# Kernel tuning notes

Hardware: AMD Instinct MI355X
Metric: run time of the kernel (lower is better)

## Reference

```python
import jax, jax.numpy as jnp
import numpy as np

NEG = -10000.0
START, STOP = 4, 5
NT = 6  # 4 emotions + START + STOP
B, T, V = 512, 2048, 100000


def setup_inputs():
    key = jax.random.key(0)
    ks = jax.random.split(key, 7)
    transitions = jax.random.normal(ks[0], (NT, NT), jnp.float32)
    transitions = transitions.at[START, :].set(NEG).at[:, STOP].set(NEG)
    weight_for_emo_shift = jax.random.normal(ks[1], (4,), jnp.float32)
    multiplier = jax.random.normal(ks[2], (4, 4), jnp.float32)
    multiplier = multiplier.at[jnp.arange(4), jnp.arange(4)].set(NEG)
    out_table = jax.random.normal(ks[3], (V, 4), jnp.float32)
    bias = jax.random.uniform(ks[4], (B, T), jnp.float32)
    sentence = jax.random.randint(ks[5], (B, T), 0, V)
    tags = jax.random.randint(ks[6], (B, T), 0, 4)
    return {"transitions": transitions, "weight_for_emo_shift": weight_for_emo_shift,
            "multiplier": multiplier, "out_table": out_table, "bias": bias,
            "sentence": sentence, "tags": tags}


def _feats(out_table, sentence):
    # sentence: [T] int -> feats [T, 6]; cols 0..3 from out_table lookup,
    # col 4 = +3 at first turn else -3, col 5 = +3 at last turn else -3.
    t = sentence.shape[0]
    emo = out_table[sentence]                                      # [T,4]
    col4 = jnp.full((t,), -3.0, out_table.dtype).at[0].set(3.0)
    col5 = jnp.full((t,), -3.0, out_table.dtype).at[t - 1].set(3.0)
    return jnp.concatenate([emo, col4[:, None], col5[:, None]], axis=1)


def _nll_one(transitions, w, M, feats, bias, tags):
    # CRF forward algorithm (log-partition) minus gold path score for one dialog.
    t = feats.shape[0]

    def step(alpha, inp):
        feat, b = inp                                              # feat [6], b scalar
        shift = b * jnp.tanh((b - 0.5) * w)                        # [4]
        te = transitions.at[:4, :4].add(M * shift[None, :])        # [next, prev]
        alpha = jax.nn.logsumexp(alpha[None, :] + te, axis=1) + feat
        return alpha, None

    alpha0 = jnp.full((NT,), NEG, feats.dtype).at[START].set(0.0)
    alphaT, _ = jax.lax.scan(step, alpha0, (feats, bias))
    fwd = jax.nn.logsumexp(alphaT + transitions[STOP])

    # gold score
    prev = jnp.concatenate([jnp.array([START], tags.dtype), tags[:-1]])
    pc = jnp.clip(prev, 0, 3)
    ar = jnp.arange(t)
    shift = bias[:, None] * jnp.tanh((bias[:, None] - 0.5) * w[None, :])  # [T,4]
    biased = shift[ar, pc] * M[tags, pc]
    use_bias = (tags < 4) & (prev < 4)
    trans_s = transitions[tags, prev] + jnp.where(use_bias, biased, 0.0)
    gold = jnp.sum(trans_s + feats[ar, tags]) + transitions[STOP, tags[-1]]
    return fwd - gold


def reference(transitions, weight_for_emo_shift, multiplier, out_table, bias, sentence, tags):
    # multiplier: softmax over dim 0, then diagonal forced to -1 (as in the
    # in-place .data mutations in the original loop).
    M = jax.nn.softmax(multiplier, axis=0)
    M = M.at[jnp.arange(4), jnp.arange(4)].set(-1.0)
    feats = jax.vmap(lambda s: _feats(out_table, s))(sentence)     # [B,T,6]
    nll = jax.vmap(lambda f, b, tg: _nll_one(transitions, weight_for_emo_shift, M, f, b, tg))(feats, bias, tags)
    return nll                                                     # [B]
```

## Files before the change

### kernel.cpp

```cpp
#include <hip/hip_runtime.h>

#define TT 2048
#define BB 512

typedef float f2 __attribute__((ext_vector_type(2)));
__device__ __forceinline__ f2 mk2(float v){ f2 r; r.x=v; r.y=v; return r; }

#if __has_builtin(__builtin_elementwise_fma)
#define FMA2(a,b,c) __builtin_elementwise_fma((a),(b),(c))
#else
#define FMA2(a,b,c) ((a)*(b)+(c))
#endif

#if __has_builtin(__builtin_amdgcn_exp2f)
__device__ __forceinline__ float fexp2(float x){ return __builtin_amdgcn_exp2f(x); }
#else
__device__ __forceinline__ float fexp2(float x){ return exp2f(x); }
#endif
#if __has_builtin(__builtin_amdgcn_logf)
__device__ __forceinline__ float flog2(float x){ return __builtin_amdgcn_logf(x); }
#else
__device__ __forceinline__ float flog2(float x){ return log2f(x); }
#endif
__device__ __forceinline__ float frcp(float x){ return __builtin_amdgcn_rcpf(x); }

#if __has_builtin(__builtin_amdgcn_cvt_pk_fp8_f32) && __has_builtin(__builtin_amdgcn_cvt_pk_f32_fp8)
__device__ __forceinline__ unsigned enc_lo(float a,float b,unsigned old){
  return (unsigned)__builtin_amdgcn_cvt_pk_fp8_f32(a,b,(int)old,false);
}
__device__ __forceinline__ unsigned enc_hi(float a,float b,unsigned old){
  return (unsigned)__builtin_amdgcn_cvt_pk_fp8_f32(a,b,(int)old,true);
}
__device__ __forceinline__ f2 dec_lo2(unsigned w){
  auto r=__builtin_amdgcn_cvt_pk_f32_fp8((int)w,false); f2 o; o.x=r[0]; o.y=r[1]; return o;
}
__device__ __forceinline__ f2 dec_hi2(unsigned w){
  auto r=__builtin_amdgcn_cvt_pk_f32_fp8((int)w,true); f2 o; o.x=r[0]; o.y=r[1]; return o;
}
#else
__device__ __forceinline__ unsigned enc1(float x){
  if (!(x > 0x1p-10f)) return 0u;
  unsigned b = __float_as_uint(x) + 0x80000u;
  int e = (int)((b>>23)&0xFF) - 127;
  if (e < -6){ int m = (int)(x*512.0f + 0.5f); return (unsigned)m; }
  if (e > 8) return 0x7Eu;
  return (unsigned)(((e+7)<<3) | ((b>>20)&7));
}
__device__ __forceinline__ float dec1(unsigned byte){
  unsigned e=(byte>>3)&0xF, m=byte&7;
  if (e==0) return (float)m * 0x1p-9f;
  return __uint_as_float(((e+120u)<<23)|(m<<20));
}
__device__ __forceinline__ unsigned enc_lo(float a,float b,unsigned old){
  return (old & 0xFFFF0000u) | enc1(a) | (enc1(b)<<8);
}
__device__ __forceinline__ unsigned enc_hi(float a,float b,unsigned old){
  return (old & 0x0000FFFFu) | (enc1(a)<<16) | (enc1(b)<<24);
}
__device__ __forceinline__ f2 dec_lo2(unsigned w){ f2 o; o.x=dec1(w&0xFF); o.y=dec1((w>>8)&0xFF); return o; }
__device__ __forceinline__ f2 dec_hi2(unsigned w){ f2 o; o.x=dec1((w>>16)&0xFF); o.y=dec1(w>>24); return o; }
#endif

__device__ __forceinline__ float lse2_4(float x0,float x1,float x2,float x3){
  float m = fmaxf(fmaxf(x0,x1),fmaxf(x2,x3));
  float e = fexp2(x0-m)+fexp2(x1-m)+fexp2(x2-m)+fexp2(x3-m);
  return m + flog2(e);
}

__global__ __launch_bounds__(256) void crf_part(
    const float* __restrict__ trans,
    const float* __restrict__ w,
    const float* __restrict__ mult,
    const float* __restrict__ out_table,
    const float* __restrict__ bias,
    const int*   __restrict__ sentence,
    const int*   __restrict__ tags,
    float* __restrict__ partM,
    float* __restrict__ partG)
{
  constexpr float INVLN2 = 1.4426950408889634f;
  const int blk = blockIdx.x;
  const int b   = blk >> 2;
  const int p   = blk & 3;
  const int tid = threadIdx.x;

  __shared__ __align__(16) char  s_te[8192];
  __shared__ float s_PAm[64*16];
  __shared__ float s_PAs[64*4];
  __shared__ float s_M[16];
  __shared__ float s_tr[36];
  __shared__ float s_wgold[4];
  float* s_PBm = (float*)s_te;
  float* s_PBs = (float*)(s_te + 4096);

  float trans2[16]; float t2max = -1e30f;
  #pragma unroll
  for (int i=0;i<4;i++)
    #pragma unroll
    for (int k=0;k<4;k++){
      float v = trans[i*6+k]*INVLN2;
      trans2[i*4+k] = v; t2max = fmaxf(t2max, v);
    }
  const float T144 = t2max + 1.4427f;

  float M[16];
  {
    int l = tid & 15;
    float mv = fexp2(mult[l]*INVLN2);
    float s1 = mv + __shfl_xor(mv, 4);
    float cs = s1 + __shfl_xor(s1, 8);
    float Ml = ((l>>2)==(l&3)) ? -1.f : mv*frcp(cs);
    if (tid < 16) s_M[tid] = Ml;
    int mi = __float_as_int(Ml);
    #pragma unroll
    for (int i=0;i<16;i++)
      M[i] = __int_as_float(__builtin_amdgcn_readlane(mi, i));
  }
  const float wc0=w[0]*2.f*INVLN2, wc1=w[1]*2.f*INVLN2,
              wc2=w[2]*2.f*INVLN2, wc3=w[3]*2.f*INVLN2;
  if (tid<36) s_tr[tid]=trans[tid];
  __syncthreads();

  float gold = 0.f;
  float cts;
  {
    const int t0    = tid<<1;
    const int gbase = b*TT + (p<<9) + t0;
    float2 bb2 = *reinterpret_cast<const float2*>(bias + gbase);
    int2  sen2 = *reinterpret_cast<const int2*>(sentence + gbase);
    int2  tg2  = *reinterpret_cast<const int2*>(tags + gbase);
    float4 ftA = *reinterpret_cast<const float4*>(out_table + (size_t)sen2.x*4);
    float4 ftB = *reinterpret_cast<const float4*>(out_table + (size_t)sen2.y*4);

    int pv0;
    if ((tid & 63)==0) pv0 = (p==0 && t0==0) ? 4 : tags[gbase-1];
    else               pv0 = __shfl_up(tg2.y, 1);

    float ctv[2];
    #pragma unroll
    for (int e=0;e<2;e++){
      const int tl = t0 + e;
      float bb   = e ? bb2.y : bb2.x;
      float4 f4e = e ? ftB   : ftA;
      int tg     = e ? tg2.y : tg2.x;
      int pv     = e ? tg2.x : pv0;

      float bh = bb-0.5f;
      float y0=fexp2(bh*wc0); float sh0=bb*(y0-1.f)*frcp(y0+1.f);
      float y1=fexp2(bh*wc1); float sh1=bb*(y1-1.f)*frcp(y1+1.f);
      float y2=fexp2(bh*wc2); float sh2v=bb*(y2-1.f)*frcp(y2+1.f);
      float y3=fexp2(bh*wc3); float sh3=bb*(y3-1.f)*frcp(y3+1.f);
      float s20=sh0*INVLN2, s21=sh1*INVLN2, s22=sh2v*INVLN2, s23=sh3*INVLN2;
      float f20=f4e.x*INVLN2, f21=f4e.y*INVLN2, f22=f4e.z*INVLN2, f23=f4e.w*INVLN2;

      float ct  = fmaxf(fmaxf(f20,f21),fmaxf(f22,f23)) + T144;
      float off = 8.0f - ct;
      float o0=f20+off, o1=f21+off, o2=f22+off, o3=f23+off;
      float a00=fexp2(fmaf(M[ 0],s20,trans2[ 0]+o0));
      float a01=fexp2(fmaf(M[ 1],s21,trans2[ 1]+o0));
      float a02=fexp2(fmaf(M[ 2],s22,trans2[ 2]+o0));
      float a03=fexp2(fmaf(M[ 3],s23,trans2[ 3]+o0));
      float a10=fexp2(fmaf(M[ 4],s20,trans2[ 4]+o1));
      float a11=fexp2(fmaf(M[ 5],s21,trans2[ 5]+o1));
      float a12=fexp2(fmaf(M[ 6],s22,trans2[ 6]+o1));
      float a13=fexp2(fmaf(M[ 7],s23,trans2[ 7]+o1));
      float a20=fexp2(fmaf(M[ 8],s20,trans2[ 8]+o2));
      float a21=fexp2(fmaf(M[ 9],s21,trans2[ 9]+o2));
      float a22=fexp2(fmaf(M[10],s22,trans2[10]+o2));
      float a23=fexp2(fmaf(M[11],s23,trans2[11]+o2));
      float a30=fexp2(fmaf(M[12],s20,trans2[12]+o3));
      float a31=fexp2(fmaf(M[13],s21,trans2[13]+o3));
      float a32=fexp2(fmaf(M[14],s22,trans2[14]+o3));
      float a33=fexp2(fmaf(M[15],s23,trans2[15]+o3));

      unsigned d0=enc_lo(a00,a10,0u); d0=enc_hi(a20,a30,d0);
      unsigned d1=enc_lo(a01,a11,0u); d1=enc_hi(a21,a31,d1);
      unsigned d2=enc_lo(a02,a12,0u); d2=enc_hi(a22,a32,d2);
      unsigned d3=enc_lo(a03,a13,0u); d3=enc_hi(a23,a33,d3);
      int g = (tl ^ ((tl>>3)&7)) << 4;
      *reinterpret_cast<uint4*>(s_te+g) = make_uint4(d0,d1,d2,d3);
      ctv[e] = ct;

      float term;
      if (pv>=4){
        term = s_tr[tg*6+4];
      } else {
        float shp=(pv==0)?sh0:(pv==1)?sh1:(pv==2)?sh2v:sh3;
        term = s_tr[tg*6+pv] + shp*s_M[tg*4+pv];
      }
      term += (tg==0)?f4e.x:(tg==1)?f4e.y:(tg==2)?f4e.z:f4e.w;
      if (p==3 && tl==511) term += s_tr[30+tg];
      gold += term;
    }
    if (p==0 && tid==0){
      *reinterpret_cast<uint4*>(s_te) = make_uint4(0x38u,0x3800u,0x380000u,0x38000000u);
      ctv[0] = 8.0f;
    }
    cts = ctv[0] + ctv[1];
  }
  #pragma unroll
  for (int off=32; off>0; off>>=1) gold += __shfl_down(gold, off);
  if ((tid & 63)==0) s_wgold[tid>>6] = gold;
  float cpair = cts + __shfl_xor(cts, 1);
  float csum  = cpair + __shfl_xor(cpair, 2);
  __syncthreads();

  {
    int c = tid>>2, j = tid&3;
    int t0c = c<<3;
    int K = c & 7;
    f2 a01, a23;
    a01.x = (j==0)?1.f:0.f; a01.y = (j==1)?1.f:0.f;
    a23.x = (j==2)?1.f:0.f; a23.y = (j==3)?1.f:0.f;
    #pragma unroll
    for (int s=0;s<8;s++){
      int g = ((t0c+s) ^ K) << 4;
      uint4 q = *reinterpret_cast<const uint4*>(s_te + g);
      float p0=a01.x, p1=a01.y, p2=a23.x, p3=a23.y;
      f2 n01 = dec_lo2(q.x)*mk2(p0);
      f2 n23 = dec_hi2(q.x)*mk2(p0);
      n01 = FMA2(dec_lo2(q.y), mk2(p1), n01);
      n23 = FMA2(dec_hi2(q.y), mk2(p1), n23);
      n01 = FMA2(dec_lo2(q.z), mk2(p2), n01);
      n23 = FMA2(dec_hi2(q.z), mk2(p2), n23);
      n01 = FMA2(dec_lo2(q.w), mk2(p3), n01);
      n23 = FMA2(dec_hi2(q.w), mk2(p3), n23);
      a01 = n01; a23 = n23;
    }
    float sum = fmaxf((a01.x+a01.y)+(a23.x+a23.y), 1e-30f);
    float inv = frcp(sum);
    float L = flog2(sum) + csum - 64.0f;
    s_PAm[c*16 + 0*4 + j] = a01.x*inv;
    s_PAm[c*16 + 1*4 + j] = a01.y*inv;
    s_PAm[c*16 + 2*4 + j] = a23.x*inv;
    s_PAm[c*16 + 3*4 + j] = a23.y*inv;
    s_PAs[c*4 + j] = L;
  }
  __syncthreads();

  if (tid < 128){
    int q = tid>>2, j = tid&3;
    const float* Am = s_PAm + (2*q)*16;
    const float* As = s_PAs + (2*q)*4;
    const float* Bm = Am + 16;
    const float* Bs = As + 4;
    float b0=Bs[0], b1=Bs[1], b2=Bs[2], b3=Bs[3];
    float m = fmaxf(fmaxf(b0,b1), fmaxf(b2,b3));
    float a0 = Am[0*4+j]*fexp2(b0-m);
    float a1 = Am[1*4+j]*fexp2(b1-m);
    float a2 = Am[2*4+j]*fexp2(b2-m);
    float a3 = Am[3*4+j]*fexp2(b3-m);
    float c0 = fmaf(Bm[ 0],a0, fmaf(Bm[ 1],a1, fmaf(Bm[ 2],a2, Bm[ 3]*a3)));
    float c1 = fmaf(Bm[ 4],a0, fmaf(Bm[ 5],a1, fmaf(Bm[ 6],a2, Bm[ 7]*a3)));
    float c2 = fmaf(Bm[ 8],a0, fmaf(Bm[ 9],a1, fmaf(Bm[10],a2, Bm[11]*a3)));
    float c3 = fmaf(Bm[12],a0, fmaf(Bm[13],a1, fmaf(Bm[14],a2, Bm[15]*a3)));
    float ssum = fmaxf((c0+c1)+(c2+c3), 1e-37f);
    float inv = frcp(ssum);
    s_PBm[q*16+0*4+j] = c0*inv;
    s_PBm[q*16+1*4+j] = c1*inv;
    s_PBm[q*16+2*4+j] = c2*inv;
    s_PBm[q*16+3*4+j] = c3*inv;
    s_PBs[q*4+j] = m + As[j] + flog2(ssum);
  }
  __syncthreads();

  if (tid < 64){
    float *srcM = s_PBm, *srcS = s_PBs, *dstM = s_PAm, *dstS = s_PAs;
    #pragma unroll 1
    for (int n=16; n>=1; n>>=1){
      if (tid < n*4){
        int q = tid>>2, j = tid&3;
        const float* Am = srcM + (2*q)*16;
        const float* As = srcS + (2*q)*4;
        const float* Bm = Am + 16;
        const float* Bs = As + 4;
        float b0=Bs[0], b1=Bs[1], b2=Bs[2], b3=Bs[3];
        float m = fmaxf(fmaxf(b0,b1), fmaxf(b2,b3));
        float a0 = Am[0*4+j]*fexp2(b0-m);
        float a1 = Am[1*4+j]*fexp2(b1-m);
        float a2 = Am[2*4+j]*fexp2(b2-m);
        float a3 = Am[3*4+j]*fexp2(b3-m);
        float c0 = fmaf(Bm[ 0],a0, fmaf(Bm[ 1],a1, fmaf(Bm[ 2],a2, Bm[ 3]*a3)));
        float c1 = fmaf(Bm[ 4],a0, fmaf(Bm[ 5],a1, fmaf(Bm[ 6],a2, Bm[ 7]*a3)));
        float c2 = fmaf(Bm[ 8],a0, fmaf(Bm[ 9],a1, fmaf(Bm[10],a2, Bm[11]*a3)));
        float c3 = fmaf(Bm[12],a0, fmaf(Bm[13],a1, fmaf(Bm[14],a2, Bm[15]*a3)));
        float ssum = fmaxf((c0+c1)+(c2+c3), 1e-37f);
        float inv = frcp(ssum);
        dstM[q*16+0*4+j] = c0*inv;
        dstM[q*16+1*4+j] = c1*inv;
        dstM[q*16+2*4+j] = c2*inv;
        dstM[q*16+3*4+j] = c3*inv;
        dstS[q*4+j] = m + As[j] + flog2(ssum);
      }
      float* tm;
      tm=srcM; srcM=dstM; dstM=tm;
      tm=srcS; srcS=dstS; dstS=tm;
    }
    const int idx = (b<<2) | p;
    if (tid < 16)      partM[idx*20 + tid] = srcM[tid];
    else if (tid < 20) partM[idx*20 + tid] = srcS[tid-16];
    if (tid == 20)
      partG[idx] = ((s_wgold[0]+s_wgold[1])+(s_wgold[2]+s_wgold[3]));
  }
}

__global__ __launch_bounds__(256) void crf_final(
    const float* __restrict__ trans,
    const float* __restrict__ out_table,
    const int*   __restrict__ sentence,
    const float* __restrict__ partM,
    const float* __restrict__ partG,
    float* __restrict__ out)
{
  constexpr float INVLN2 = 1.4426950408889634f;
  constexpr float LN2    = 0.6931471805599453f;
  const int tid = threadIdx.x;
  const int j   = tid & 3;
  const int dd  = tid >> 2;
  const int d   = (blockIdx.x<<6) + dd;

  __shared__ float s_m[64][21];

  const float* P0 = partM + (size_t)(d<<2)*20;
  float c0=P0[0+j], c1=P0[4+j], c2=P0[8+j], c3=P0[12+j];
  float Lc=P0[16+j];
  #pragma unroll
  for (int q=1;q<4;q++){
    const float* Bq = partM + (size_t)((d<<2)+q)*20;
    float b0=Bq[16], b1=Bq[17], b2=Bq[18], b3=Bq[19];
    float m = fmaxf(fmaxf(b0,b1), fmaxf(b2,b3));
    float a0=c0*fexp2(b0-m), a1=c1*fexp2(b1-m),
          a2=c2*fexp2(b2-m), a3=c3*fexp2(b3-m);
    float n0 = fmaf(Bq[ 0],a0, fmaf(Bq[ 1],a1, fmaf(Bq[ 2],a2, Bq[ 3]*a3)));
    float n1 = fmaf(Bq[ 4],a0, fmaf(Bq[ 5],a1, fmaf(Bq[ 6],a2, Bq[ 7]*a3)));
    float n2 = fmaf(Bq[ 8],a0, fmaf(Bq[ 9],a1, fmaf(Bq[10],a2, Bq[11]*a3)));
    float n3 = fmaf(Bq[12],a0, fmaf(Bq[13],a1, fmaf(Bq[14],a2, Bq[15]*a3)));
    float ss = fmaxf((n0+n1)+(n2+n3), 1e-37f);
    float iv = frcp(ss);
    c0=n0*iv; c1=n1*iv; c2=n2*iv; c3=n3*iv;
    Lc += m + flog2(ss);
  }
  s_m[dd][0+j]=c0; s_m[dd][4+j]=c1; s_m[dd][8+j]=c2; s_m[dd][12+j]=c3;
  s_m[dd][16+j]=Lc;
  __syncthreads();

  if (j==0){
    const float* Pf = s_m[dd];
    const float* Ls = s_m[dd]+16;
    int s0 = sentence[(size_t)d*TT];
    float4 f0 = *reinterpret_cast<const float4*>(out_table + (size_t)s0*4);
    float a0 = (trans[ 4] + f0.x)*INVLN2;
    float a1 = (trans[10] + f0.y)*INVLN2;
    float a2 = (trans[16] + f0.z)*INVLN2;
    float a3 = (trans[22] + f0.w)*INVLN2;
    float u0 = Ls[0]+a0, u1 = Ls[1]+a1, u2 = Ls[2]+a2, u3 = Ls[3]+a3;
    float m2 = fmaxf(fmaxf(u0,u1), fmaxf(u2,u3));
    float e0 = fexp2(u0-m2), e1 = fexp2(u1-m2), e2 = fexp2(u2-m2), e3 = fexp2(u3-m2);
    float v0 = fmaf(Pf[ 0],e0, fmaf(Pf[ 1],e1, fmaf(Pf[ 2],e2, Pf[ 3]*e3)));
    float v1 = fmaf(Pf[ 4],e0, fmaf(Pf[ 5],e1, fmaf(Pf[ 6],e2, Pf[ 7]*e3)));
    float v2 = fmaf(Pf[ 8],e0, fmaf(Pf[ 9],e1, fmaf(Pf[10],e2, Pf[11]*e3)));
    float v3 = fmaf(Pf[12],e0, fmaf(Pf[13],e1, fmaf(Pf[14],e2, Pf[15]*e3)));
    float n0 = flog2(v0)+m2, n1 = flog2(v1)+m2, n2 = flog2(v2)+m2, n3 = flog2(v3)+m2;
    float fwd2 = lse2_4(n0+trans[30]*INVLN2, n1+trans[31]*INVLN2,
                        n2+trans[32]*INVLN2, n3+trans[33]*INVLN2);
    const float* Gp = partG + (size_t)(d<<2);
    float g = (Gp[0]+Gp[1])+(Gp[2]+Gp[3]);
    out[d] = fwd2*LN2 - g;
  }
}

extern "C" void kernel_launch(void* const* d_in, const int* in_sizes, int n_in,
                              void* d_out, int out_size, void* d_ws, size_t ws_size,
                              hipStream_t stream) {
  const float* trans     = (const float*)d_in[0];
  const float* w         = (const float*)d_in[1];
  const float* mult      = (const float*)d_in[2];
  const float* out_table = (const float*)d_in[3];
  const float* bias      = (const float*)d_in[4];
  const int*   sentence  = (const int*)d_in[5];
  const int*   tags      = (const int*)d_in[6];
  float* partM = (float*)d_ws;
  float* partG = (float*)((char*)d_ws + BB*4*20*sizeof(float));
  crf_part<<<BB*4, 256, 0, stream>>>(trans, w, mult, out_table, bias, sentence, tags,
                                     partM, partG);
  crf_final<<<BB/64, 256, 0, stream>>>(trans, out_table, sentence, partM, partG,
                                       (float*)d_out);
}
```

Measured before the change: 21.22 us.

## Fuse partial and final CRF kernels into one 1024-thread block per dialog

Replaces the two-kernel scheme (four 256-thread blocks per dialog writing partial matrices to workspace, then a final combine kernel) with a single kernel using one 1024-thread block per sequence. The whole 2048-step scan is reduced in shared memory by a tree of 4x4 matrix combines, and the final logsumexp and gold sum are done in-block. This removes the second launch and the global round-trip of partials. In exchange each block is larger, uses more shared memory (about 52KB), and the grid shrinks to 512 blocks, which may lower occupancy and parallelism.

```diff
diff --git a/kernel.cpp b/kernel.cpp
--- a/kernel.cpp
+++ b/kernel.cpp
@@ -67,7 +67,7 @@
   return m + flog2(e);
 }
 
-__global__ __launch_bounds__(256) void crf_part(
+__global__ __launch_bounds__(1024) void crf_kernel(
     const float* __restrict__ trans,
     const float* __restrict__ w,
     const float* __restrict__ mult,
@@ -75,23 +75,21 @@
     const float* __restrict__ bias,
     const int*   __restrict__ sentence,
     const int*   __restrict__ tags,
-    float* __restrict__ partM,
-    float* __restrict__ partG)
+    float* __restrict__ out)
 {
   constexpr float INVLN2 = 1.4426950408889634f;
-  const int blk = blockIdx.x;
-  const int b   = blk >> 2;
-  const int p   = blk & 3;
+  constexpr float LN2    = 0.6931471805599453f;
+  const int b   = blockIdx.x;
   const int tid = threadIdx.x;
 
-  __shared__ __align__(16) char  s_te[8192];
-  __shared__ float s_PAm[64*16];
-  __shared__ float s_PAs[64*4];
+  __shared__ __align__(16) char  s_te[32768];
+  __shared__ float s_PAm[256*16];
+  __shared__ float s_PAs[256*4];
   __shared__ float s_M[16];
   __shared__ float s_tr[36];
-  __shared__ float s_wgold[4];
+  __shared__ float s_wgold[16];
   float* s_PBm = (float*)s_te;
-  float* s_PBs = (float*)(s_te + 4096);
+  float* s_PBs = (float*)(s_te + 16384);
 
   float trans2[16]; float t2max = -1e30f;
   #pragma unroll
@@ -125,7 +123,7 @@
   float cts;
   {
     const int t0    = tid<<1;
-    const int gbase = b*TT + (p<<9) + t0;
+    const int gbase = b*TT + t0;
     float2 bb2 = *reinterpret_cast<const float2*>(bias + gbase);
     int2  sen2 = *reinterpret_cast<const int2*>(sentence + gbase);
     int2  tg2  = *reinterpret_cast<const int2*>(tags + gbase);
@@ -133,7 +131,7 @@
     float4 ftB = *reinterpret_cast<const float4*>(out_table + (size_t)sen2.y*4);
 
     int pv0;
-    if ((tid & 63)==0) pv0 = (p==0 && t0==0) ? 4 : tags[gbase-1];
+    if ((tid & 63)==0) pv0 = (t0==0) ? 4 : tags[gbase-1];
     else               pv0 = __shfl_up(tg2.y, 1);
 
     float ctv[2];
@@ -189,10 +187,10 @@
         term = s_tr[tg*6+pv] + shp*s_M[tg*4+pv];
       }
       term += (tg==0)?f4e.x:(tg==1)?f4e.y:(tg==2)?f4e.z:f4e.w;
-      if (p==3 && tl==511) term += s_tr[30+tg];
+      if (tl==TT-1) term += s_tr[30+tg];
       gold += term;
     }
-    if (p==0 && tid==0){
+    if (tid==0){
       *reinterpret_cast<uint4*>(s_te) = make_uint4(0x38u,0x3800u,0x380000u,0x38000000u);
       ctv[0] = 8.0f;
     }
@@ -238,134 +236,69 @@
   }
   __syncthreads();
 
-  if (tid < 128){
-    int q = tid>>2, j = tid&3;
-    const float* Am = s_PAm + (2*q)*16;
-    const float* As = s_PAs + (2*q)*4;
-    const float* Bm = Am + 16;
-    const float* Bs = As + 4;
-    float b0=Bs[0], b1=Bs[1], b2=Bs[2], b3=Bs[3];
-    float m = fmaxf(fmaxf(b0,b1), fmaxf(b2,b3));
-    float a0 = Am[0*4+j]*fexp2(b0-m);
-    float a1 = Am[1*4+j]*fexp2(b1-m);
-    float a2 = Am[2*4+j]*fexp2(b2-m);
-    float a3 = Am[3*4+j]*fexp2(b3-m);
-    float c0 = fmaf(Bm[ 0],a0, fmaf(Bm[ 1],a1, fmaf(Bm[ 2],a2, Bm[ 3]*a3)));
-    float c1 = fmaf(Bm[ 4],a0, fmaf(Bm[ 5],a1, fmaf(Bm[ 6],a2, Bm[ 7]*a3)));
-    float c2 = fmaf(Bm[ 8],a0, fmaf(Bm[ 9],a1, fmaf(Bm[10],a2, Bm[11]*a3)));
-    float c3 = fmaf(Bm[12],a0, fmaf(Bm[13],a1, fmaf(Bm[14],a2, Bm[15]*a3)));
-    float ssum = fmaxf((c0+c1)+(c2+c3), 1e-37f);
-    float inv = frcp(ssum);
-    s_PBm[q*16+0*4+j] = c0*inv;
-    s_PBm[q*16+1*4+j] = c1*inv;
-    s_PBm[q*16+2*4+j] = c2*inv;
-    s_PBm[q*16+3*4+j] = c3*inv;
-    s_PBs[q*4+j] = m + As[j] + flog2(ssum);
-  }
+  #define COMBINE(SRC_M,SRC_S,DST_M,DST_S,Q,J)                                   \
+    { const float* Am = (SRC_M) + (2*(Q))*16;                                    \
+      const float* As = (SRC_S) + (2*(Q))*4;                                     \
+      const float* Bm = Am + 16;                                                 \
+      const float* Bs = As + 4;                                                  \
+      float b0=Bs[0], b1=Bs[1], b2=Bs[2], b3=Bs[3];                              \
+      float m = fmaxf(fmaxf(b0,b1), fmaxf(b2,b3));                               \
+      float a0 = Am[0*4+(J)]*fexp2(b0-m);                                        \
+      float a1 = Am[1*4+(J)]*fexp2(b1-m);                                        \
+      float a2 = Am[2*4+(J)]*fexp2(b2-m);                                        \
+      float a3 = Am[3*4+(J)]*fexp2(b3-m);                                        \
+      float c0 = fmaf(Bm[ 0],a0, fmaf(Bm[ 1],a1, fmaf(Bm[ 2],a2, Bm[ 3]*a3)));  \
+      float c1 = fmaf(Bm[ 4],a0, fmaf(Bm[ 5],a1, fmaf(Bm[ 6],a2, Bm[ 7]*a3)));  \
+      float c2 = fmaf(Bm[ 8],a0, fmaf(Bm[ 9],a1, fmaf(Bm[10],a2, Bm[11]*a3)));  \
+      float c3 = fmaf(Bm[12],a0, fmaf(Bm[13],a1, fmaf(Bm[14],a2, Bm[15]*a3)));  \
+      float ssum = fmaxf((c0+c1)+(c2+c3), 1e-37f);                               \
+      float inv = frcp(ssum);                                                    \
+      (DST_M)[(Q)*16+0*4+(J)] = c0*inv;                                          \
+      (DST_M)[(Q)*16+1*4+(J)] = c1*inv;                                          \
+      (DST_M)[(Q)*16+2*4+(J)] = c2*inv;                                          \
+      (DST_M)[(Q)*16+3*4+(J)] = c3*inv;                                          \
+      (DST_S)[(Q)*4+(J)] = m + As[(J)] + flog2(ssum); }
+
+  if (tid < 512) COMBINE(s_PAm, s_PAs, s_PBm, s_PBs, (tid>>2), (tid&3));
+  __syncthreads();
+  if (tid < 256) COMBINE(s_PBm, s_PBs, s_PAm, s_PAs, (tid>>2), (tid&3));
+  __syncthreads();
+  if (tid < 128) COMBINE(s_PAm, s_PAs, s_PBm, s_PBs, (tid>>2), (tid&3));
   __syncthreads();
 
   if (tid < 64){
     float *srcM = s_PBm, *srcS = s_PBs, *dstM = s_PAm, *dstS = s_PAs;
     #pragma unroll 1
     for (int n=16; n>=1; n>>=1){
-      if (tid < n*4){
-        int q = tid>>2, j = tid&3;
-        const float* Am = srcM + (2*q)*16;
-        const float* As = srcS + (2*q)*4;
-        const float* Bm = Am + 16;
-        const float* Bs = As + 4;
-        float b0=Bs[0], b1=Bs[1], b2=Bs[2], b3=Bs[3];
-        float m = fmaxf(fmaxf(b0,b1), fmaxf(b2,b3));
-        float a0 = Am[0*4+j]*fexp2(b0-m);
-        float a1 = Am[1*4+j]*fexp2(b1-m);
-        float a2 = Am[2*4+j]*fexp2(b2-m);
-        float a3 = Am[3*4+j]*fexp2(b3-m);
-        float c0 = fmaf(Bm[ 0],a0, fmaf(Bm[ 1],a1, fmaf(Bm[ 2],a2, Bm[ 3]*a3)));
-        float c1 = fmaf(Bm[ 4],a0, fmaf(Bm[ 5],a1, fmaf(Bm[ 6],a2, Bm[ 7]*a3)));
-        float c2 = fmaf(Bm[ 8],a0, fmaf(Bm[ 9],a1, fmaf(Bm[10],a2, Bm[11]*a3)));
-        float c3 = fmaf(Bm[12],a0, fmaf(Bm[13],a1, fmaf(Bm[14],a2, Bm[15]*a3)));
-        float ssum = fmaxf((c0+c1)+(c2+c3), 1e-37f);
-        float inv = frcp(ssum);
-        dstM[q*16+0*4+j] = c0*inv;
-        dstM[q*16+1*4+j] = c1*inv;
-        dstM[q*16+2*4+j] = c2*inv;
-        dstM[q*16+3*4+j] = c3*inv;
-        dstS[q*4+j] = m + As[j] + flog2(ssum);
-      }
+      if (tid < n*4) COMBINE(srcM, srcS, dstM, dstS, (tid>>2), (tid&3));
       float* tm;
       tm=srcM; srcM=dstM; dstM=tm;
       tm=srcS; srcS=dstS; dstS=tm;
     }
-    const int idx = (b<<2) | p;
-    if (tid < 16)      partM[idx*20 + tid] = srcM[tid];
-    else if (tid < 20) partM[idx*20 + tid] = srcS[tid-16];
-    if (tid == 20)
-      partG[idx] = ((s_wgold[0]+s_wgold[1])+(s_wgold[2]+s_wgold[3]));
-  }
-}
-
-__global__ __launch_bounds__(256) void crf_final(
-    const float* __restrict__ trans,
-    const float* __restrict__ out_table,
-    const int*   __restrict__ sentence,
-    const float* __restrict__ partM,
-    const float* __restrict__ partG,
-    float* __restrict__ out)
-{
-  constexpr float INVLN2 = 1.4426950408889634f;
-  constexpr float LN2    = 0.6931471805599453f;
-  const int tid = threadIdx.x;
-  const int j   = tid & 3;
-  const int dd  = tid >> 2;
-  const int d   = (blockIdx.x<<6) + dd;
-
-  __shared__ float s_m[64][21];
-
-  const float* P0 = partM + (size_t)(d<<2)*20;
-  float c0=P0[0+j], c1=P0[4+j], c2=P0[8+j], c3=P0[12+j];
-  float Lc=P0[16+j];
-  #pragma unroll
-  for (int q=1;q<4;q++){
-    const float* Bq = partM + (size_t)((d<<2)+q)*20;
-    float b0=Bq[16], b1=Bq[17], b2=Bq[18], b3=Bq[19];
-    float m = fmaxf(fmaxf(b0,b1), fmaxf(b2,b3));
-    float a0=c0*fexp2(b0-m), a1=c1*fexp2(b1-m),
-          a2=c2*fexp2(b2-m), a3=c3*fexp2(b3-m);
-    float n0 = fmaf(Bq[ 0],a0, fmaf(Bq[ 1],a1, fmaf(Bq[ 2],a2, Bq[ 3]*a3)));
-    float n1 = fmaf(Bq[ 4],a0, fmaf(Bq[ 5],a1, fmaf(Bq[ 6],a2, Bq[ 7]*a3)));
-    float n2 = fmaf(Bq[ 8],a0, fmaf(Bq[ 9],a1, fmaf(Bq[10],a2, Bq[11]*a3)));
-    float n3 = fmaf(Bq[12],a0, fmaf(Bq[13],a1, fmaf(Bq[14],a2, Bq[15]*a3)));
-    float ss = fmaxf((n0+n1)+(n2+n3), 1e-37f);
-    float iv = frcp(ss);
-    c0=n0*iv; c1=n1*iv; c2=n2*iv; c3=n3*iv;
-    Lc += m + flog2(ss);
-  }
-  s_m[dd][0+j]=c0; s_m[dd][4+j]=c1; s_m[dd][8+j]=c2; s_m[dd][12+j]=c3;
-  s_m[dd][16+j]=Lc;
-  __syncthreads();
-
-  if (j==0){
-    const float* Pf = s_m[dd];
-    const float* Ls = s_m[dd]+16;
-    int s0 = sentence[(size_t)d*TT];
-    float4 f0 = *reinterpret_cast<const float4*>(out_table + (size_t)s0*4);
-    float a0 = (trans[ 4] + f0.x)*INVLN2;
-    float a1 = (trans[10] + f0.y)*INVLN2;
-    float a2 = (trans[16] + f0.z)*INVLN2;
-    float a3 = (trans[22] + f0.w)*INVLN2;
-    float u0 = Ls[0]+a0, u1 = Ls[1]+a1, u2 = Ls[2]+a2, u3 = Ls[3]+a3;
-    float m2 = fmaxf(fmaxf(u0,u1), fmaxf(u2,u3));
-    float e0 = fexp2(u0-m2), e1 = fexp2(u1-m2), e2 = fexp2(u2-m2), e3 = fexp2(u3-m2);
-    float v0 = fmaf(Pf[ 0],e0, fmaf(Pf[ 1],e1, fmaf(Pf[ 2],e2, Pf[ 3]*e3)));
-    float v1 = fmaf(Pf[ 4],e0, fmaf(Pf[ 5],e1, fmaf(Pf[ 6],e2, Pf[ 7]*e3)));
-    float v2 = fmaf(Pf[ 8],e0, fmaf(Pf[ 9],e1, fmaf(Pf[10],e2, Pf[11]*e3)));
-    float v3 = fmaf(Pf[12],e0, fmaf(Pf[13],e1, fmaf(Pf[14],e2, Pf[15]*e3)));
-    float n0 = flog2(v0)+m2, n1 = flog2(v1)+m2, n2 = flog2(v2)+m2, n3 = flog2(v3)+m2;
-    float fwd2 = lse2_4(n0+trans[30]*INVLN2, n1+trans[31]*INVLN2,
-                        n2+trans[32]*INVLN2, n3+trans[33]*INVLN2);
-    const float* Gp = partG + (size_t)(d<<2);
-    float g = (Gp[0]+Gp[1])+(Gp[2]+Gp[3]);
-    out[d] = fwd2*LN2 - g;
+    if (tid==0){
+      const float* Pf = srcM;
+      const float* Ls = srcS;
+      int s0 = sentence[(size_t)b*TT];
+      float4 f0 = *reinterpret_cast<const float4*>(out_table + (size_t)s0*4);
+      float a0 = (s_tr[ 4] + f0.x)*INVLN2;
+      float a1 = (s_tr[10] + f0.y)*INVLN2;
+      float a2 = (s_tr[16] + f0.z)*INVLN2;
+      float a3 = (s_tr[22] + f0.w)*INVLN2;
+      float u0 = Ls[0]+a0, u1 = Ls[1]+a1, u2 = Ls[2]+a2, u3 = Ls[3]+a3;
+      float m2 = fmaxf(fmaxf(u0,u1), fmaxf(u2,u3));
+      float e0 = fexp2(u0-m2), e1 = fexp2(u1-m2), e2 = fexp2(u2-m2), e3 = fexp2(u3-m2);
+      float v0 = fmaf(Pf[ 0],e0, fmaf(Pf[ 1],e1, fmaf(Pf[ 2],e2, Pf[ 3]*e3)));
+      float v1 = fmaf(Pf[ 4],e0, fmaf(Pf[ 5],e1, fmaf(Pf[ 6],e2, Pf[ 7]*e3)));
+      float v2 = fmaf(Pf[ 8],e0, fmaf(Pf[ 9],e1, fmaf(Pf[10],e2, Pf[11]*e3)));
+      float v3 = fmaf(Pf[12],e0, fmaf(Pf[13],e1, fmaf(Pf[14],e2, Pf[15]*e3)));
+      float n0 = flog2(v0)+m2, n1 = flog2(v1)+m2, n2 = flog2(v2)+m2, n3 = flog2(v3)+m2;
+      float fwd2 = lse2_4(n0+s_tr[30]*INVLN2, n1+s_tr[31]*INVLN2,
+                          n2+s_tr[32]*INVLN2, n3+s_tr[33]*INVLN2);
+      float g = 0.f;
+      #pragma unroll
+      for (int i=0;i<16;i++) g += s_wgold[i];
+      out[b] = fwd2*LN2 - g;
+    }
   }
 }
 
@@ -379,10 +312,6 @@
   const float* bias      = (const float*)d_in[4];
   const int*   sentence  = (const int*)d_in[5];
   const int*   tags      = (const int*)d_in[6];
-  float* partM = (float*)d_ws;
-  float* partG = (float*)((char*)d_ws + BB*4*20*sizeof(float));
-  crf_part<<<BB*4, 256, 0, stream>>>(trans, w, mult, out_table, bias, sentence, tags,
-                                     partM, partG);
-  crf_final<<<BB/64, 256, 0, stream>>>(trans, out_table, sentence, partM, partG,
-                                       (float*)d_out);
-}
+  crf_kernel<<<BB, 1024, 0, stream>>>(trans, w, mult, out_table, bias, sentence, tags,
+                                      (float*)d_out);
+}
```

After: 19.78 us. 1.07x faster.
